# Performance work log

Measured on AMD Instinct MI355X. Metric: run time of the kernel, lower is better.

## Reference

```python
import jax, jax.numpy as jnp
import numpy as np

B, TQ, TK, E, H, DH = 4, 1024, 1024, 1024, 16, 64
EPS = 1e-5

def setup_inputs() -> dict:
    key = jax.random.key(0)
    ks = jax.random.split(key, 16)
    s = 0.02
    return {
        "x": jax.random.normal(ks[0], (B, TQ, E), jnp.float32),
        "encoder_out": jax.random.normal(ks[1], (B, TK, E), jnp.float32),
        "Q1w": jax.random.normal(ks[2], (H, DH, E), jnp.float32) * s,
        "Q1b": jax.random.normal(ks[3], (H, DH), jnp.float32) * s,
        "Q2w": jax.random.normal(ks[4], (H, DH, E), jnp.float32) * s,
        "Q2b": jax.random.normal(ks[5], (H, DH), jnp.float32) * s,
        "K1w": jax.random.normal(ks[6], (H, DH, E), jnp.float32) * s,
        "K1b": jax.random.normal(ks[7], (H, DH), jnp.float32) * s,
        "K2w": jax.random.normal(ks[8], (H, DH, E), jnp.float32) * s,
        "K2b": jax.random.normal(ks[9], (H, DH), jnp.float32) * s,
        "Vw": jax.random.normal(ks[10], (H, DH, E), jnp.float32) * s,
        "Vb": jax.random.normal(ks[11], (H, DH), jnp.float32) * s,
        "lam": jax.random.uniform(ks[12], (H,), jnp.float32, 0.5, 1.0),
        "gn_gamma": jnp.ones((H * DH,), jnp.float32),
        "gn_beta": jnp.zeros((H * DH,), jnp.float32),
        "out_w": jax.random.normal(ks[13], (E, H * DH), jnp.float32) * s,
        "out_b": jax.random.normal(ks[14], (E,), jnp.float32) * s,
    }

def _proj(inp, w, b):
    # inp: [B,T,E], w: [H,DH,E] -> [B,H,T,DH]
    return jnp.einsum('bte,hde->bhtd', inp, w) + b[None, :, None, :]

def reference(x, encoder_out, Q1w, Q1b, Q2w, Q2b, K1w, K1b, K2w, K2b, Vw, Vb,
              lam, gn_gamma, gn_beta, out_w, out_b):
    scale = 1.0 / jnp.sqrt(jnp.float32(DH))
    q1 = _proj(x, Q1w, Q1b)
    q2 = _proj(x, Q2w, Q2b)
    k1 = _proj(encoder_out, K1w, K1b)
    k2 = _proj(encoder_out, K2w, K2b)
    v = _proj(encoder_out, Vw, Vb)
    s1 = jnp.einsum('bhtd,bhsd->bhts', q1, k1) * scale  # [B,H,TQ,TK]
    s2 = jnp.einsum('bhtd,bhsd->bhts', q2, k2) * scale
    w = jax.nn.softmax(s1, axis=-1) - lam[None, :, None, None] * jax.nn.softmax(s2, axis=-1)
    out = jnp.einsum('bhts,bhsd->bhtd', w, v)  # [B,H,TQ,DH]
    # GroupNorm(num_groups=H, channels=H*DH) over [B,C,T]: per (B,H) stats over (T,DH)
    mu = jnp.mean(out, axis=(2, 3), keepdims=True)
    var = jnp.mean(jnp.square(out - mu), axis=(2, 3), keepdims=True)
    normed = (out - mu) * jax.lax.rsqrt(var + EPS)
    g = gn_gamma.reshape(H, DH)[None, :, None, :]
    b_ = gn_beta.reshape(H, DH)[None, :, None, :]
    normed = normed * g + b_
    y = normed.transpose(0, 2, 1, 3).reshape(B, TQ, H * DH)
    return y @ out_w.T + out_b
```

## Files before the change

kernel.cpp:

```cpp
#include <hip/hip_runtime.h>
#include <cmath>

typedef __bf16 bf16_t;
typedef bf16_t bf16x8 __attribute__((ext_vector_type(8)));
typedef bf16_t bf16x4 __attribute__((ext_vector_type(4)));
typedef float  f32x4  __attribute__((ext_vector_type(4)));

#define Bn  4
#define TQn 1024
#define TKn 1024
#define En  1024
#define Hn  16
#define DHn 64

static constexpr float EPSv = 1e-5f;
static constexpr float C_SCALE = 0.18033688011112042f;

#define GLDS16(g, l)                                                         \
    __builtin_amdgcn_global_load_lds(                                        \
        (const __attribute__((address_space(1))) void*)(g),                  \
        (__attribute__((address_space(3))) void*)(l), 16, 0, 0)

__global__ __launch_bounds__(256)
void cvt_all(const float* __restrict__ x, const float* __restrict__ enc,
             const float* __restrict__ q1w, const float* __restrict__ q2w,
             const float* __restrict__ k1w, const float* __restrict__ k2w,
             const float* __restrict__ vw,  const float* __restrict__ outw,
             bf16_t* __restrict__ xb, bf16_t* __restrict__ encb,
             bf16_t* __restrict__ wq, bf16_t* __restrict__ wkv,
             bf16_t* __restrict__ wob)
{
    int idx = blockIdx.x * 256 + threadIdx.x;
    const float* src; bf16_t* dst;
    if      (idx < 1048576) { src = x    + (size_t)idx * 4;              dst = xb   + (size_t)idx * 4; }
    else if (idx < 2097152) { src = enc  + (size_t)(idx - 1048576) * 4;  dst = encb + (size_t)(idx - 1048576) * 4; }
    else if (idx < 2359296) { src = q1w  + (size_t)(idx - 2097152) * 4;  dst = wq   + (size_t)(idx - 2097152) * 4; }
    else if (idx < 2621440) { src = q2w  + (size_t)(idx - 2359296) * 4;  dst = wq   + 1048576 + (size_t)(idx - 2359296) * 4; }
    else if (idx < 2883584) { src = k1w  + (size_t)(idx - 2621440) * 4;  dst = wkv  + (size_t)(idx - 2621440) * 4; }
    else if (idx < 3145728) { src = k2w  + (size_t)(idx - 2883584) * 4;  dst = wkv  + 1048576 + (size_t)(idx - 2883584) * 4; }
    else if (idx < 3407872) { src = vw   + (size_t)(idx - 3145728) * 4;  dst = wkv  + 2097152 + (size_t)(idx - 3145728) * 4; }
    else                    { src = outw + (size_t)(idx - 3407872) * 4;  dst = wob  + (size_t)(idx - 3407872) * 4; }
    float4 v = *(const float4*)src;
    bf16x4 o;
    o[0] = (bf16_t)v.x; o[1] = (bf16_t)v.y; o[2] = (bf16_t)v.z; o[3] = (bf16_t)v.w;
    *(bf16x4*)dst = o;
}

template<int OUTMODE, int BN>
__device__ __forceinline__
void gemm_core(const bf16_t* __restrict__ A, const bf16_t* __restrict__ W,
               const float* __restrict__ bp, void* __restrict__ Cout,
               int K, int blockM, int blockN,
               bf16_t* __restrict__ sA, bf16_t* __restrict__ sB)
{
    constexpr int NJ = BN / 32;
    constexpr int CB = BN / 32;
    const int tid = threadIdx.x;
    const int w = tid >> 6, lane = tid & 63;
    const int q = lane >> 4, r = lane & 15;
    const int wm = w & 1, wn = w >> 1;

    f32x4 acc[4][NJ];
#pragma unroll
    for (int i = 0; i < 4; ++i)
#pragma unroll
        for (int j = 0; j < NJ; ++j) acc[i][j] = (f32x4){0.f, 0.f, 0.f, 0.f};

    for (int k0 = 0; k0 < K; k0 += 64) {
#pragma unroll
        for (int c = 0; c < 4; ++c) {
            const int s = c * 256 + tid;
            const int row = s >> 3;
            const int cg = (s & 7) ^ (row & 7);
            GLDS16(A + (size_t)(blockM + row) * K + k0 + cg * 8, sA + c * 2048 + w * 512);
            if (c < CB)
                GLDS16(W + (size_t)(blockN + row) * K + k0 + cg * 8, sB + c * 2048 + w * 512);
        }
        __syncthreads();
#pragma unroll
        for (int ks = 0; ks < 2; ++ks) {
            bf16x8 a[4], b[NJ];
#pragma unroll
            for (int i = 0; i < 4; ++i) {
                const int row = wm * 64 + i * 16 + r;
                const int g = (ks * 4 + q) ^ (row & 7);
                a[i] = *(const bf16x8*)&sA[row * 64 + g * 8];
            }
#pragma unroll
            for (int j = 0; j < NJ; ++j) {
                const int row = wn * (BN / 2) + j * 16 + r;
                const int g = (ks * 4 + q) ^ (row & 7);
                b[j] = *(const bf16x8*)&sB[row * 64 + g * 8];
            }
#pragma unroll
            for (int i = 0; i < 4; ++i)
#pragma unroll
                for (int j = 0; j < NJ; ++j)
                    acc[i][j] = __builtin_amdgcn_mfma_f32_16x16x32_bf16(a[i], b[j], acc[i][j], 0, 0, 0);
        }
        __syncthreads();
    }

    const int seg = blockN >> 10;
#pragma unroll
    for (int j = 0; j < NJ; ++j) {
        const int n = blockN + wn * (BN / 2) + j * 16 + r;
        const float bv = bp[n & 1023];
#pragma unroll
        for (int i = 0; i < 4; ++i) {
            f32x4 v = acc[i][j];
#pragma unroll
            for (int e = 0; e < 4; ++e) {
                const int m = blockM + wm * 64 + i * 16 + q * 4 + e;
                const float val = v[e] + bv;
                if (OUTMODE == 0) {
                    const int bb = m >> 10, t = m & 1023;
                    const int h = (n >> 6) & 15, d = n & 63;
                    ((bf16_t*)Cout)[((((size_t)seg * 4 + bb) * 16 + h) * 1024 + t) * 64 + d] = (bf16_t)val;
                } else {
                    ((float*)Cout)[(size_t)m * 1024 + n] = val;
                }
            }
        }
    }
}

__global__ __launch_bounds__(256, 3)
void gemm_proj(const bf16_t* __restrict__ xb, const bf16_t* __restrict__ encb,
               const bf16_t* __restrict__ wq, const bf16_t* __restrict__ wkv,
               const float* __restrict__ q1b, const float* __restrict__ q2b,
               const float* __restrict__ k1b, const float* __restrict__ k2b,
               const float* __restrict__ vb,
               bf16_t* __restrict__ q12, bf16_t* __restrict__ k12v)
{
    __shared__ bf16_t sA[128 * 64];
    __shared__ bf16_t sB[128 * 64];
    int bx = blockIdx.x;
    const bf16_t* A; const bf16_t* W; bf16_t* C; const float* bp; int blockN;
    if (bx < 16) {
        A = xb; W = wq; C = q12; blockN = bx << 7;
        bp = (blockN >> 10) ? q2b : q1b;
    } else {
        bx -= 16;
        A = encb; W = wkv; C = k12v; blockN = bx << 7;
        const int seg = blockN >> 10;
        bp = (seg == 0) ? k1b : ((seg == 1) ? k2b : vb);
    }
    gemm_core<0, 128>(A, W, bp, C, 1024, blockIdx.y << 7, blockN, sA, sB);
}

__global__ __launch_bounds__(256, 3)
void gemm_out(const bf16_t* __restrict__ yb, const bf16_t* __restrict__ wob,
              const float* __restrict__ outb, float* __restrict__ out)
{
    __shared__ bf16_t sA[128 * 64];
    __shared__ bf16_t sB[64 * 64];
    gemm_core<1, 64>(yb, wob, outb, out, 1024, blockIdx.y << 7, blockIdx.x << 6, sA, sB);
}

__device__ __forceinline__ void compute_S(const bf16_t* __restrict__ sK,
                                          const bf16x8 (&fQ)[2][2],
                                          f32x4 (&S)[4][2], int q, int r)
{
#pragma unroll
    for (int i = 0; i < 4; ++i)
#pragma unroll
        for (int j = 0; j < 2; ++j) S[i][j] = (f32x4){0.f, 0.f, 0.f, 0.f};
#pragma unroll
    for (int ks = 0; ks < 2; ++ks) {
        bf16x8 fK[4];
#pragma unroll
        for (int i = 0; i < 4; ++i) {
            const int row = i * 16 + r;
            const int g = (ks * 4 + q) ^ (row & 7);
            fK[i] = *(const bf16x8*)&sK[row * 64 + g * 8];
        }
        __builtin_amdgcn_s_setprio(1);
#pragma unroll
        for (int i = 0; i < 4; ++i)
#pragma unroll
            for (int j = 0; j < 2; ++j)
                S[i][j] = __builtin_amdgcn_mfma_f32_16x16x32_bf16(fK[i], fQ[j][ks], S[i][j], 0, 0, 0);
        __builtin_amdgcn_s_setprio(0);
    }
}

__device__ __forceinline__ void softmax_pw(f32x4 (&S)[4][2], bf16_t* __restrict__ sPt,
                                           float (&l)[2], int w, int q, int r)
{
#pragma unroll
    for (int j = 0; j < 2; ++j) {
        const int t = w * 32 + j * 16 + r;
        float part = 0.f;
#pragma unroll
        for (int i = 0; i < 4; ++i) {
            bf16x4 pk;
#pragma unroll
            for (int e = 0; e < 4; ++e) {
                const float p = __builtin_amdgcn_exp2f(S[i][j][e] * C_SCALE);
                part += p;
                pk[e] = (bf16_t)p;
            }
            const int sb = i * 16 + q * 4;
            const int g = (sb >> 3) ^ (t & 7);
            *(bf16x4*)&sPt[t * 64 + g * 8 + (sb & 7)] = pk;
        }
        l[j] += part;
    }
}

__device__ __forceinline__ void pv(const bf16_t* __restrict__ sPt,
                                   const bf16x8 (&fV)[4][2],
                                   f32x4 (&O)[2][4], int w, int q, int r)
{
#pragma unroll
    for (int ks = 0; ks < 2; ++ks) {
        bf16x8 fP[2];
#pragma unroll
        for (int i2 = 0; i2 < 2; ++i2) {
            const int m = w * 32 + i2 * 16 + r;
            const int g = (ks * 4 + q) ^ (m & 7);
            fP[i2] = *(const bf16x8*)&sPt[m * 64 + g * 8];
        }
        __builtin_amdgcn_s_setprio(1);
#pragma unroll
        for (int i2 = 0; i2 < 2; ++i2)
#pragma unroll
            for (int j = 0; j < 4; ++j)
                O[i2][j] = __builtin_amdgcn_mfma_f32_16x16x32_bf16(fP[i2], fV[j][ks], O[i2][j], 0, 0, 0);
        __builtin_amdgcn_s_setprio(0);
    }
}

__global__ __launch_bounds__(256, 2)
void diff_attn_mfma(const bf16_t* __restrict__ q12, const bf16_t* __restrict__ k12v,
                    const float* __restrict__ lam, bf16_t* __restrict__ out,
                    float* __restrict__ stats)
{
    __shared__ bf16_t sK1[2][64 * 64];
    __shared__ bf16_t sK2[2][64 * 64];
    __shared__ bf16_t sVt[64 * 64];
    __shared__ bf16_t sPt1[128 * 64];
    __shared__ bf16_t sPt2[128 * 64];
    __shared__ float  sl1[128], sl2[128];
    __shared__ float  sred[16];

    const int tid = threadIdx.x;
    const int w = tid >> 6, lane = tid & 63;
    const int q = lane >> 4, r = lane & 15;
    const int bh = blockIdx.x, qt = blockIdx.y;
    const float lamv = lam[bh & (Hn - 1)];

    const size_t HT = (size_t)TKn * DHn;
    const bf16_t* q1g = q12 + (size_t)bh * HT + (size_t)qt * 128 * DHn;
    const bf16_t* q2g = q1g + 64 * HT;
    const bf16_t* k1g = k12v + (size_t)bh * HT;
    const bf16_t* k2g = k1g + 64 * HT;
    const bf16_t* vg  = k1g + 128 * HT;

    bf16x8 fQ1[2][2], fQ2[2][2];
#pragma unroll
    for (int j = 0; j < 2; ++j) {
        const int t = w * 32 + j * 16 + r;
#pragma unroll
        for (int ks = 0; ks < 2; ++ks) {
            fQ1[j][ks] = *(const bf16x8*)(q1g + (size_t)t * 64 + ks * 32 + q * 8);
            fQ2[j][ks] = *(const bf16x8*)(q2g + (size_t)t * 64 + ks * 32 + q * 8);
        }
    }

    f32x4 O1[2][4], O2[2][4];
    float l1[2] = {0.f, 0.f}, l2[2] = {0.f, 0.f};
#pragma unroll
    for (int i = 0; i < 2; ++i)
#pragma unroll
        for (int j = 0; j < 4; ++j) { O1[i][j] = (f32x4){0.f,0.f,0.f,0.f}; O2[i][j] = (f32x4){0.f,0.f,0.f,0.f}; }

    {
#pragma unroll
        for (int c = 0; c < 2; ++c) {
            const int s = c * 256 + tid;
            const int row = s >> 3;
            const int cg = (s & 7) ^ (row & 7);
            GLDS16(k1g + row * 64 + cg * 8, &sK1[0][c * 2048 + w * 512]);
            GLDS16(k2g + row * 64 + cg * 8, &sK2[0][c * 2048 + w * 512]);
        }
        bf16x8 v0[2];
#pragma unroll
        for (int rep = 0; rep < 2; ++rep)
            v0[rep] = *(const bf16x8*)(vg + (size_t)lane * 64 + (w * 2 + rep) * 8);
        __syncthreads();
#pragma unroll
        for (int rep = 0; rep < 2; ++rep) {
            const int d0 = (w * 2 + rep) * 8;
#pragma unroll
            for (int i = 0; i < 8; ++i) {
                const int d = d0 + i;
                sVt[d * 64 + (((lane >> 3) ^ i) << 3) + (lane & 7)] = v0[rep][i];
            }
        }
        __syncthreads();
    }

    bf16x8 vr[2];
    for (int st = 0; st < TKn / 64; ++st) {
        const int cur = st & 1;
        if (st < 15) {
            const bf16_t* k1p = k1g + (size_t)(st + 1) * 4096;
            const bf16_t* k2p = k2g + (size_t)(st + 1) * 4096;
#pragma unroll
            for (int c = 0; c < 2; ++c) {
                const int s = c * 256 + tid;
                const int row = s >> 3;
                const int cg = (s & 7) ^ (row & 7);
                GLDS16(k1p + row * 64 + cg * 8, &sK1[cur ^ 1][c * 2048 + w * 512]);
                GLDS16(k2p + row * 64 + cg * 8, &sK2[cur ^ 1][c * 2048 + w * 512]);
            }
            const bf16_t* vp = vg + (size_t)(st + 1) * 4096;
#pragma unroll
            for (int rep = 0; rep < 2; ++rep)
                vr[rep] = *(const bf16x8*)(vp + (size_t)lane * 64 + (w * 2 + rep) * 8);
        }

        {
            f32x4 S[4][2];
            compute_S(sK1[cur], fQ1, S, q, r);
            softmax_pw(S, sPt1, l1, w, q, r);
        }
        {
            f32x4 S[4][2];
            compute_S(sK2[cur], fQ2, S, q, r);
            softmax_pw(S, sPt2, l2, w, q, r);
        }
        bf16x8 fV[4][2];
#pragma unroll
        for (int j = 0; j < 4; ++j)
#pragma unroll
            for (int ks = 0; ks < 2; ++ks) {
                const int d = j * 16 + r;
                const int g = (ks * 4 + q) ^ (d & 7);
                fV[j][ks] = *(const bf16x8*)&sVt[d * 64 + g * 8];
            }
        pv(sPt1, fV, O1, w, q, r);
        pv(sPt2, fV, O2, w, q, r);

        __syncthreads();
        if (st < 15) {
#pragma unroll
            for (int rep = 0; rep < 2; ++rep) {
                const int d0 = (w * 2 + rep) * 8;
#pragma unroll
                for (int i = 0; i < 8; ++i) {
                    const int d = d0 + i;
                    sVt[d * 64 + (((lane >> 3) ^ i) << 3) + (lane & 7)] = vr[rep][i];
                }
            }
            __syncthreads();
        }
    }

#pragma unroll
    for (int j = 0; j < 2; ++j) {
        float v1 = l1[j];
        v1 += __shfl_xor(v1, 16); v1 += __shfl_xor(v1, 32);
        float v2 = l2[j];
        v2 += __shfl_xor(v2, 16); v2 += __shfl_xor(v2, 32);
        if (q == 0) { sl1[w * 32 + j * 16 + r] = v1; sl2[w * 32 + j * 16 + r] = v2; }
    }

    bf16_t* op = out + ((size_t)bh * TQn + (size_t)qt * 128) * DHn;
    float ssum = 0.f, ssq = 0.f;
#pragma unroll
    for (int i2 = 0; i2 < 2; ++i2)
#pragma unroll
        for (int e = 0; e < 4; ++e) {
            const int t = w * 32 + i2 * 16 + q * 4 + e;
            const float inv1 = 1.0f / sl1[t];
            const float inv2 = lamv / sl2[t];
#pragma unroll
            for (int j = 0; j < 4; ++j) {
                const float o = O1[i2][j][e] * inv1 - O2[i2][j][e] * inv2;
                op[(size_t)t * 64 + j * 16 + r] = (bf16_t)o;
                ssum += o;
                ssq += o * o;
            }
        }
#pragma unroll
    for (int d = 1; d < 64; d <<= 1) {
        ssum += __shfl_xor(ssum, d);
        ssq  += __shfl_xor(ssq, d);
    }
    if (lane == 0) { sred[w] = ssum; sred[8 + w] = ssq; }
    __syncthreads();
    if (tid == 0) {
        stats[(bh << 3) + qt]       = sred[0] + sred[1] + sred[2] + sred[3];
        stats[512 + (bh << 3) + qt] = sred[8] + sred[9] + sred[10] + sred[11];
    }
}

__global__ __launch_bounds__(256)
void gn_apply(const bf16_t* __restrict__ attn, const float* __restrict__ stats,
              const float* __restrict__ gamma, const float* __restrict__ beta,
              bf16_t* __restrict__ y)
{
    const int f = blockIdx.x * 256 + threadIdx.x;
    const int d8 = (f & 7) << 3;
    const int t  = (f >> 3) & 1023;
    const int bh = f >> 13;
    const int h  = bh & 15;
    const int b  = bh >> 4;
    const float* p1 = stats + (bh << 3);
    const float* p2 = stats + 512 + (bh << 3);
    float s1 = 0.f, s2 = 0.f;
#pragma unroll
    for (int k = 0; k < 8; ++k) { s1 += p1[k]; s2 += p2[k]; }
    const float mu = s1 * (1.f / 65536.f);
    const float var = s2 * (1.f / 65536.f) - mu * mu;
    const float rstd = rsqrtf(var + EPSv);
    bf16x8 v = *(const bf16x8*)&attn[((size_t)bh << 16) + t * 64 + d8];
    const int c = h * 64 + d8;
    const float* gp = gamma + c;
    const float* bp = beta + c;
    bf16x8 o;
#pragma unroll
    for (int i = 0; i < 8; ++i)
        o[i] = (bf16_t)(((float)v[i] - mu) * rstd * gp[i] + bp[i]);
    *(bf16x8*)&y[((size_t)(b * 1024 + t)) * 1024 + c] = o;
}

extern "C" void kernel_launch(void* const* d_in, const int* in_sizes, int n_in,
                              void* d_out, int out_size, void* d_ws, size_t ws_size,
                              hipStream_t stream)
{
    const float* x    = (const float*)d_in[0];
    const float* enc  = (const float*)d_in[1];
    const float* Q1w  = (const float*)d_in[2];
    const float* Q1b  = (const float*)d_in[3];
    const float* Q2w  = (const float*)d_in[4];
    const float* Q2b  = (const float*)d_in[5];
    const float* K1w  = (const float*)d_in[6];
    const float* K1b  = (const float*)d_in[7];
    const float* K2w  = (const float*)d_in[8];
    const float* K2b  = (const float*)d_in[9];
    const float* Vw   = (const float*)d_in[10];
    const float* Vb   = (const float*)d_in[11];
    const float* lam  = (const float*)d_in[12];
    const float* gng  = (const float*)d_in[13];
    const float* gnb  = (const float*)d_in[14];
    const float* outw = (const float*)d_in[15];
    const float* outb = (const float*)d_in[16];
    float* out = (float*)d_out;

    bf16_t* xb   = (bf16_t*)d_ws;
    bf16_t* encb = xb   + 4194304;
    bf16_t* wq   = encb + 4194304;
    bf16_t* wkv  = wq   + 2097152;
    bf16_t* wob  = wkv  + 3145728;
    bf16_t* q12  = wob  + 1048576;
    bf16_t* k12v = q12  + 8388608;
    bf16_t* attnb= xb;
    bf16_t* yb   = encb;
    float*  stats= (float*)wq;

    cvt_all<<<14336, 256, 0, stream>>>(x, enc, Q1w, Q2w, K1w, K2w, Vw, outw,
                                       xb, encb, wq, wkv, wob);

    gemm_proj<<<dim3(40, 32), 256, 0, stream>>>(xb, encb, wq, wkv,
                                                Q1b, Q2b, K1b, K2b, Vb, q12, k12v);

    diff_attn_mfma<<<dim3(64, 8), 256, 0, stream>>>(q12, k12v, lam, attnb, stats);

    gn_apply<<<2048, 256, 0, stream>>>(attnb, stats, gng, gnb, yb);

    gemm_out<<<dim3(16, 32), 256, 0, stream>>>(yb, wob, outb, out);
}
```

Measured before the change: 252.3 us.

## Use 512-thread attention blocks, shared P buffer, and remapped 64x128 output GEMM

The attention kernel moves to 8 waves per block, each owning 16 query rows, and interleaves S, softmax and PV per branch so a single P buffer in LDS is reused by both branches. The output GEMM switches to 64x128 tiles with a 1-D grid whose block index is remapped so neighbouring blocks on each XCD share A rows, and its occupancy hint rises to 4. The generic gemm_core template is inlined into each kernel. The aim is more waves in flight, less LDS use and better L2 locality. The cost is half the MFMA work per wave in attention and extra synchronisation overhead per block.

```diff
diff --git a/kernel.cpp b/kernel.cpp
--- a/kernel.cpp
+++ b/kernel.cpp
@@ -46,85 +46,6 @@
     *(bf16x4*)dst = o;
 }
 
-template<int OUTMODE, int BN>
-__device__ __forceinline__
-void gemm_core(const bf16_t* __restrict__ A, const bf16_t* __restrict__ W,
-               const float* __restrict__ bp, void* __restrict__ Cout,
-               int K, int blockM, int blockN,
-               bf16_t* __restrict__ sA, bf16_t* __restrict__ sB)
-{
-    constexpr int NJ = BN / 32;
-    constexpr int CB = BN / 32;
-    const int tid = threadIdx.x;
-    const int w = tid >> 6, lane = tid & 63;
-    const int q = lane >> 4, r = lane & 15;
-    const int wm = w & 1, wn = w >> 1;
-
-    f32x4 acc[4][NJ];
-#pragma unroll
-    for (int i = 0; i < 4; ++i)
-#pragma unroll
-        for (int j = 0; j < NJ; ++j) acc[i][j] = (f32x4){0.f, 0.f, 0.f, 0.f};
-
-    for (int k0 = 0; k0 < K; k0 += 64) {
-#pragma unroll
-        for (int c = 0; c < 4; ++c) {
-            const int s = c * 256 + tid;
-            const int row = s >> 3;
-            const int cg = (s & 7) ^ (row & 7);
-            GLDS16(A + (size_t)(blockM + row) * K + k0 + cg * 8, sA + c * 2048 + w * 512);
-            if (c < CB)
-                GLDS16(W + (size_t)(blockN + row) * K + k0 + cg * 8, sB + c * 2048 + w * 512);
-        }
-        __syncthreads();
-#pragma unroll
-        for (int ks = 0; ks < 2; ++ks) {
-            bf16x8 a[4], b[NJ];
-#pragma unroll
-            for (int i = 0; i < 4; ++i) {
-                const int row = wm * 64 + i * 16 + r;
-                const int g = (ks * 4 + q) ^ (row & 7);
-                a[i] = *(const bf16x8*)&sA[row * 64 + g * 8];
-            }
-#pragma unroll
-            for (int j = 0; j < NJ; ++j) {
-                const int row = wn * (BN / 2) + j * 16 + r;
-                const int g = (ks * 4 + q) ^ (row & 7);
-                b[j] = *(const bf16x8*)&sB[row * 64 + g * 8];
-            }
-#pragma unroll
-            for (int i = 0; i < 4; ++i)
-#pragma unroll
-                for (int j = 0; j < NJ; ++j)
-                    acc[i][j] = __builtin_amdgcn_mfma_f32_16x16x32_bf16(a[i], b[j], acc[i][j], 0, 0, 0);
-        }
-        __syncthreads();
-    }
-
-    const int seg = blockN >> 10;
-#pragma unroll
-    for (int j = 0; j < NJ; ++j) {
-        const int n = blockN + wn * (BN / 2) + j * 16 + r;
-        const float bv = bp[n & 1023];
-#pragma unroll
-        for (int i = 0; i < 4; ++i) {
-            f32x4 v = acc[i][j];
-#pragma unroll
-            for (int e = 0; e < 4; ++e) {
-                const int m = blockM + wm * 64 + i * 16 + q * 4 + e;
-                const float val = v[e] + bv;
-                if (OUTMODE == 0) {
-                    const int bb = m >> 10, t = m & 1023;
-                    const int h = (n >> 6) & 15, d = n & 63;
-                    ((bf16_t*)Cout)[((((size_t)seg * 4 + bb) * 16 + h) * 1024 + t) * 64 + d] = (bf16_t)val;
-                } else {
-                    ((float*)Cout)[(size_t)m * 1024 + n] = val;
-                }
-            }
-        }
-    }
-}
-
 __global__ __launch_bounds__(256, 3)
 void gemm_proj(const bf16_t* __restrict__ xb, const bf16_t* __restrict__ encb,
                const bf16_t* __restrict__ wq, const bf16_t* __restrict__ wkv,
@@ -146,26 +67,156 @@
         const int seg = blockN >> 10;
         bp = (seg == 0) ? k1b : ((seg == 1) ? k2b : vb);
     }
-    gemm_core<0, 128>(A, W, bp, C, 1024, blockIdx.y << 7, blockN, sA, sB);
-}
-
-__global__ __launch_bounds__(256, 3)
+    const int blockM = blockIdx.y << 7;
+
+    const int tid = threadIdx.x;
+    const int w = tid >> 6, lane = tid & 63;
+    const int q = lane >> 4, r = lane & 15;
+    const int wm = w & 1, wn = w >> 1;
+
+    f32x4 acc[4][4];
+#pragma unroll
+    for (int i = 0; i < 4; ++i)
+#pragma unroll
+        for (int j = 0; j < 4; ++j) acc[i][j] = (f32x4){0.f, 0.f, 0.f, 0.f};
+
+    for (int k0 = 0; k0 < 1024; k0 += 64) {
+#pragma unroll
+        for (int c = 0; c < 4; ++c) {
+            const int s = c * 256 + tid;
+            const int row = s >> 3;
+            const int cg = (s & 7) ^ (row & 7);
+            GLDS16(A + (size_t)(blockM + row) * 1024 + k0 + cg * 8, sA + c * 2048 + w * 512);
+            GLDS16(W + (size_t)(blockN + row) * 1024 + k0 + cg * 8, sB + c * 2048 + w * 512);
+        }
+        __syncthreads();
+#pragma unroll
+        for (int ks = 0; ks < 2; ++ks) {
+            bf16x8 a[4], b[4];
+#pragma unroll
+            for (int i = 0; i < 4; ++i) {
+                const int row = wm * 64 + i * 16 + r;
+                const int g = (ks * 4 + q) ^ (row & 7);
+                a[i] = *(const bf16x8*)&sA[row * 64 + g * 8];
+            }
+#pragma unroll
+            for (int j = 0; j < 4; ++j) {
+                const int row = wn * 64 + j * 16 + r;
+                const int g = (ks * 4 + q) ^ (row & 7);
+                b[j] = *(const bf16x8*)&sB[row * 64 + g * 8];
+            }
+#pragma unroll
+            for (int i = 0; i < 4; ++i)
+#pragma unroll
+                for (int j = 0; j < 4; ++j)
+                    acc[i][j] = __builtin_amdgcn_mfma_f32_16x16x32_bf16(a[i], b[j], acc[i][j], 0, 0, 0);
+        }
+        __syncthreads();
+    }
+
+    const int seg = blockN >> 10;
+#pragma unroll
+    for (int j = 0; j < 4; ++j) {
+        const int n = blockN + wn * 64 + j * 16 + r;
+        const float bv = bp[n & 1023];
+#pragma unroll
+        for (int i = 0; i < 4; ++i) {
+            f32x4 v = acc[i][j];
+#pragma unroll
+            for (int e = 0; e < 4; ++e) {
+                const int m = blockM + wm * 64 + i * 16 + q * 4 + e;
+                const float val = v[e] + bv;
+                const int bb = m >> 10, t = m & 1023;
+                const int h = (n >> 6) & 15, d = n & 63;
+                ((bf16_t*)C)[((((size_t)seg * 4 + bb) * 16 + h) * 1024 + t) * 64 + d] = (bf16_t)val;
+            }
+        }
+    }
+}
+
+__global__ __launch_bounds__(256, 4)
 void gemm_out(const bf16_t* __restrict__ yb, const bf16_t* __restrict__ wob,
               const float* __restrict__ outb, float* __restrict__ out)
 {
-    __shared__ bf16_t sA[128 * 64];
-    __shared__ bf16_t sB[64 * 64];
-    gemm_core<1, 64>(yb, wob, outb, out, 1024, blockIdx.y << 7, blockIdx.x << 6, sA, sB);
+    __shared__ bf16_t sA[64 * 64];
+    __shared__ bf16_t sB[128 * 64];
+    const int L = blockIdx.x;
+    const int xcd = L & 7, kk = L >> 3;
+    const int blockM = (xcd * 8 + (kk >> 3)) * 64;
+    const int blockN = (kk & 7) * 128;
+
+    const int tid = threadIdx.x;
+    const int w = tid >> 6, lane = tid & 63;
+    const int q = lane >> 4, r = lane & 15;
+
+    f32x4 acc[4][2];
+#pragma unroll
+    for (int i = 0; i < 4; ++i)
+#pragma unroll
+        for (int j = 0; j < 2; ++j) acc[i][j] = (f32x4){0.f, 0.f, 0.f, 0.f};
+
+    for (int k0 = 0; k0 < 1024; k0 += 64) {
+#pragma unroll
+        for (int c = 0; c < 2; ++c) {
+            const int s = c * 256 + tid;
+            const int row = s >> 3;
+            const int cg = (s & 7) ^ (row & 7);
+            GLDS16(yb + (size_t)(blockM + row) * 1024 + k0 + cg * 8, sA + c * 2048 + w * 512);
+        }
+#pragma unroll
+        for (int c = 0; c < 4; ++c) {
+            const int s = c * 256 + tid;
+            const int row = s >> 3;
+            const int cg = (s & 7) ^ (row & 7);
+            GLDS16(wob + (size_t)(blockN + row) * 1024 + k0 + cg * 8, sB + c * 2048 + w * 512);
+        }
+        __syncthreads();
+#pragma unroll
+        for (int ks = 0; ks < 2; ++ks) {
+            bf16x8 a[4], b[2];
+#pragma unroll
+            for (int i = 0; i < 4; ++i) {
+                const int row = i * 16 + r;
+                const int g = (ks * 4 + q) ^ (row & 7);
+                a[i] = *(const bf16x8*)&sA[row * 64 + g * 8];
+            }
+#pragma unroll
+            for (int j = 0; j < 2; ++j) {
+                const int row = w * 32 + j * 16 + r;
+                const int g = (ks * 4 + q) ^ (row & 7);
+                b[j] = *(const bf16x8*)&sB[row * 64 + g * 8];
+            }
+#pragma unroll
+            for (int i = 0; i < 4; ++i)
+#pragma unroll
+                for (int j = 0; j < 2; ++j)
+                    acc[i][j] = __builtin_amdgcn_mfma_f32_16x16x32_bf16(a[i], b[j], acc[i][j], 0, 0, 0);
+        }
+        __syncthreads();
+    }
+
+#pragma unroll
+    for (int j = 0; j < 2; ++j) {
+        const int n = blockN + w * 32 + j * 16 + r;
+        const float bv = outb[n];
+#pragma unroll
+        for (int i = 0; i < 4; ++i) {
+            f32x4 v = acc[i][j];
+#pragma unroll
+            for (int e = 0; e < 4; ++e) {
+                const int m = blockM + i * 16 + q * 4 + e;
+                out[(size_t)m * 1024 + n] = v[e] + bv;
+            }
+        }
+    }
 }
 
 __device__ __forceinline__ void compute_S(const bf16_t* __restrict__ sK,
-                                          const bf16x8 (&fQ)[2][2],
-                                          f32x4 (&S)[4][2], int q, int r)
-{
-#pragma unroll
-    for (int i = 0; i < 4; ++i)
-#pragma unroll
-        for (int j = 0; j < 2; ++j) S[i][j] = (f32x4){0.f, 0.f, 0.f, 0.f};
+                                          const bf16x8 (&fQ)[2],
+                                          f32x4 (&S)[4], int q, int r)
+{
+#pragma unroll
+    for (int i = 0; i < 4; ++i) S[i] = (f32x4){0.f, 0.f, 0.f, 0.f};
 #pragma unroll
     for (int ks = 0; ks < 2; ++ks) {
         bf16x8 fK[4];
@@ -178,61 +229,50 @@
         __builtin_amdgcn_s_setprio(1);
 #pragma unroll
         for (int i = 0; i < 4; ++i)
-#pragma unroll
-            for (int j = 0; j < 2; ++j)
-                S[i][j] = __builtin_amdgcn_mfma_f32_16x16x32_bf16(fK[i], fQ[j][ks], S[i][j], 0, 0, 0);
+            S[i] = __builtin_amdgcn_mfma_f32_16x16x32_bf16(fK[i], fQ[ks], S[i], 0, 0, 0);
         __builtin_amdgcn_s_setprio(0);
     }
 }
 
-__device__ __forceinline__ void softmax_pw(f32x4 (&S)[4][2], bf16_t* __restrict__ sPt,
-                                           float (&l)[2], int w, int q, int r)
-{
-#pragma unroll
-    for (int j = 0; j < 2; ++j) {
-        const int t = w * 32 + j * 16 + r;
-        float part = 0.f;
-#pragma unroll
-        for (int i = 0; i < 4; ++i) {
-            bf16x4 pk;
-#pragma unroll
-            for (int e = 0; e < 4; ++e) {
-                const float p = __builtin_amdgcn_exp2f(S[i][j][e] * C_SCALE);
-                part += p;
-                pk[e] = (bf16_t)p;
-            }
-            const int sb = i * 16 + q * 4;
-            const int g = (sb >> 3) ^ (t & 7);
-            *(bf16x4*)&sPt[t * 64 + g * 8 + (sb & 7)] = pk;
-        }
-        l[j] += part;
-    }
+__device__ __forceinline__ void softmax_pw(f32x4 (&S)[4], bf16_t* __restrict__ sPt,
+                                           float& l, int w, int q, int r)
+{
+    const int t = w * 16 + r;
+    float part = 0.f;
+#pragma unroll
+    for (int i = 0; i < 4; ++i) {
+        bf16x4 pk;
+#pragma unroll
+        for (int e = 0; e < 4; ++e) {
+            const float p = __builtin_amdgcn_exp2f(S[i][e] * C_SCALE);
+            part += p;
+            pk[e] = (bf16_t)p;
+        }
+        const int sb = i * 16 + q * 4;
+        const int g = (sb >> 3) ^ (t & 7);
+        *(bf16x4*)&sPt[t * 64 + g * 8 + (sb & 7)] = pk;
+    }
+    l += part;
 }
 
 __device__ __forceinline__ void pv(const bf16_t* __restrict__ sPt,
                                    const bf16x8 (&fV)[4][2],
-                                   f32x4 (&O)[2][4], int w, int q, int r)
+                                   f32x4 (&O)[4], int w, int q, int r)
 {
 #pragma unroll
     for (int ks = 0; ks < 2; ++ks) {
-        bf16x8 fP[2];
-#pragma unroll
-        for (int i2 = 0; i2 < 2; ++i2) {
-            const int m = w * 32 + i2 * 16 + r;
-            const int g = (ks * 4 + q) ^ (m & 7);
-            fP[i2] = *(const bf16x8*)&sPt[m * 64 + g * 8];
-        }
+        const int m = w * 16 + r;
+        const int g = (ks * 4 + q) ^ (m & 7);
+        bf16x8 fP = *(const bf16x8*)&sPt[m * 64 + g * 8];
         __builtin_amdgcn_s_setprio(1);
 #pragma unroll
-        for (int i2 = 0; i2 < 2; ++i2)
-#pragma unroll
-            for (int j = 0; j < 4; ++j)
-                O[i2][j] = __builtin_amdgcn_mfma_f32_16x16x32_bf16(fP[i2], fV[j][ks], O[i2][j], 0, 0, 0);
+        for (int j = 0; j < 4; ++j)
+            O[j] = __builtin_amdgcn_mfma_f32_16x16x32_bf16(fP, fV[j][ks], O[j], 0, 0, 0);
         __builtin_amdgcn_s_setprio(0);
     }
 }
 
-__global__ __launch_bounds__(256, 2)
+__global__ __launch_bounds__(512, 2)
 void diff_attn_mfma(const bf16_t* __restrict__ q12, const bf16_t* __restrict__ k12v,
                     const float* __restrict__ lam, bf16_t* __restrict__ out,
                     float* __restrict__ stats)
@@ -240,8 +280,7 @@
     __shared__ bf16_t sK1[2][64 * 64];
     __shared__ bf16_t sK2[2][64 * 64];
     __shared__ bf16_t sVt[64 * 64];
-    __shared__ bf16_t sPt1[128 * 64];
-    __shared__ bf16_t sPt2[128 * 64];
+    __shared__ bf16_t sPt[128 * 64];
     __shared__ float  sl1[128], sl2[128];
     __shared__ float  sred[16];
 
@@ -258,80 +297,47 @@
     const bf16_t* k2g = k1g + 64 * HT;
     const bf16_t* vg  = k1g + 128 * HT;
 
-    bf16x8 fQ1[2][2], fQ2[2][2];
-#pragma unroll
-    for (int j = 0; j < 2; ++j) {
-        const int t = w * 32 + j * 16 + r;
+    bf16x8 fQ1[2], fQ2[2];
+    {
+        const int t = w * 16 + r;
 #pragma unroll
         for (int ks = 0; ks < 2; ++ks) {
-            fQ1[j][ks] = *(const bf16x8*)(q1g + (size_t)t * 64 + ks * 32 + q * 8);
-            fQ2[j][ks] = *(const bf16x8*)(q2g + (size_t)t * 64 + ks * 32 + q * 8);
-        }
-    }
-
-    f32x4 O1[2][4], O2[2][4];
-    float l1[2] = {0.f, 0.f}, l2[2] = {0.f, 0.f};
-#pragma unroll
-    for (int i = 0; i < 2; ++i)
-#pragma unroll
-        for (int j = 0; j < 4; ++j) { O1[i][j] = (f32x4){0.f,0.f,0.f,0.f}; O2[i][j] = (f32x4){0.f,0.f,0.f,0.f}; }
+            fQ1[ks] = *(const bf16x8*)(q1g + (size_t)t * 64 + ks * 32 + q * 8);
+            fQ2[ks] = *(const bf16x8*)(q2g + (size_t)t * 64 + ks * 32 + q * 8);
+        }
+    }
+
+    f32x4 O1[4], O2[4];
+    float l1 = 0.f, l2 = 0.f;
+#pragma unroll
+    for (int j = 0; j < 4; ++j) { O1[j] = (f32x4){0.f,0.f,0.f,0.f}; O2[j] = (f32x4){0.f,0.f,0.f,0.f}; }
 
     {
-#pragma unroll
-        for (int c = 0; c < 2; ++c) {
-            const int s = c * 256 + tid;
-            const int row = s >> 3;
-            const int cg = (s & 7) ^ (row & 7);
-            GLDS16(k1g + row * 64 + cg * 8, &sK1[0][c * 2048 + w * 512]);
-            GLDS16(k2g + row * 64 + cg * 8, &sK2[0][c * 2048 + w * 512]);
-        }
-        bf16x8 v0[2];
-#pragma unroll
-        for (int rep = 0; rep < 2; ++rep)
-            v0[rep] = *(const bf16x8*)(vg + (size_t)lane * 64 + (w * 2 + rep) * 8);
-        __syncthreads();
-#pragma unroll
-        for (int rep = 0; rep < 2; ++rep) {
-            const int d0 = (w * 2 + rep) * 8;
-#pragma unroll
-            for (int i = 0; i < 8; ++i) {
-                const int d = d0 + i;
-                sVt[d * 64 + (((lane >> 3) ^ i) << 3) + (lane & 7)] = v0[rep][i];
-            }
-        }
-        __syncthreads();
-    }
-
-    bf16x8 vr[2];
+        const int row = tid >> 3;
+        const int cg = (tid & 7) ^ (row & 7);
+        GLDS16(k1g + row * 64 + cg * 8, &sK1[0][tid * 8]);
+        GLDS16(k2g + row * 64 + cg * 8, &sK2[0][tid * 8]);
+        const int s = tid & 63;
+        bf16x8 v0 = *(const bf16x8*)(vg + (size_t)s * 64 + w * 8);
+#pragma unroll
+        for (int i = 0; i < 8; ++i) {
+            const int d = w * 8 + i;
+            sVt[d * 64 + (((s >> 3) ^ i) << 3) + (s & 7)] = v0[i];
+        }
+        __syncthreads();
+    }
+
+    bf16x8 vr;
     for (int st = 0; st < TKn / 64; ++st) {
         const int cur = st & 1;
         if (st < 15) {
-            const bf16_t* k1p = k1g + (size_t)(st + 1) * 4096;
-            const bf16_t* k2p = k2g + (size_t)(st + 1) * 4096;
-#pragma unroll
-            for (int c = 0; c < 2; ++c) {
-                const int s = c * 256 + tid;
-                const int row = s >> 3;
-                const int cg = (s & 7) ^ (row & 7);
-                GLDS16(k1p + row * 64 + cg * 8, &sK1[cur ^ 1][c * 2048 + w * 512]);
-                GLDS16(k2p + row * 64 + cg * 8, &sK2[cur ^ 1][c * 2048 + w * 512]);
-            }
-            const bf16_t* vp = vg + (size_t)(st + 1) * 4096;
-#pragma unroll
-            for (int rep = 0; rep < 2; ++rep)
-                vr[rep] = *(const bf16x8*)(vp + (size_t)lane * 64 + (w * 2 + rep) * 8);
-        }
-
-        {
-            f32x4 S[4][2];
-            compute_S(sK1[cur], fQ1, S, q, r);
-            softmax_pw(S, sPt1, l1, w, q, r);
-        }
-        {
-            f32x4 S[4][2];
-            compute_S(sK2[cur], fQ2, S, q, r);
-            softmax_pw(S, sPt2, l2, w, q, r);
-        }
+            const int row = tid >> 3;
+            const int cg = (tid & 7) ^ (row & 7);
+            GLDS16(k1g + (size_t)(st + 1) * 4096 + row * 64 + cg * 8, &sK1[cur ^ 1][tid * 8]);
+            GLDS16(k2g + (size_t)(st + 1) * 4096 + row * 64 + cg * 8, &sK2[cur ^ 1][tid * 8]);
+            vr = *(const bf16x8*)(vg + (size_t)(st + 1) * 4096 + (size_t)(tid & 63) * 64 + w * 8);
+        }
+
         bf16x8 fV[4][2];
 #pragma unroll
         for (int j = 0; j < 4; ++j)
@@ -341,50 +347,54 @@
                 const int g = (ks * 4 + q) ^ (d & 7);
                 fV[j][ks] = *(const bf16x8*)&sVt[d * 64 + g * 8];
             }
-        pv(sPt1, fV, O1, w, q, r);
-        pv(sPt2, fV, O2, w, q, r);
+        {
+            f32x4 S[4];
+            compute_S(sK1[cur], fQ1, S, q, r);
+            softmax_pw(S, sPt, l1, w, q, r);
+            pv(sPt, fV, O1, w, q, r);
+        }
+        {
+            f32x4 S[4];
+            compute_S(sK2[cur], fQ2, S, q, r);
+            softmax_pw(S, sPt, l2, w, q, r);
+            pv(sPt, fV, O2, w, q, r);
+        }
 
         __syncthreads();
         if (st < 15) {
-#pragma unroll
-            for (int rep = 0; rep < 2; ++rep) {
-                const int d0 = (w * 2 + rep) * 8;
-#pragma unroll
-                for (int i = 0; i < 8; ++i) {
-                    const int d = d0 + i;
-                    sVt[d * 64 + (((lane >> 3) ^ i) << 3) + (lane & 7)] = vr[rep][i];
-                }
+            const int s = tid & 63;
+#pragma unroll
+            for (int i = 0; i < 8; ++i) {
+                const int d = w * 8 + i;
+                sVt[d * 64 + (((s >> 3) ^ i) << 3) + (s & 7)] = vr[i];
             }
             __syncthreads();
         }
     }
 
-#pragma unroll
-    for (int j = 0; j < 2; ++j) {
-        float v1 = l1[j];
+    {
+        float v1 = l1;
         v1 += __shfl_xor(v1, 16); v1 += __shfl_xor(v1, 32);
-        float v2 = l2[j];
+        float v2 = l2;
         v2 += __shfl_xor(v2, 16); v2 += __shfl_xor(v2, 32);
-        if (q == 0) { sl1[w * 32 + j * 16 + r] = v1; sl2[w * 32 + j * 16 + r] = v2; }
+        if (q == 0) { sl1[w * 16 + r] = v1; sl2[w * 16 + r] = v2; }
     }
 
     bf16_t* op = out + ((size_t)bh * TQn + (size_t)qt * 128) * DHn;
     float ssum = 0.f, ssq = 0.f;
 #pragma unroll
-    for (int i2 = 0; i2 < 2; ++i2)
-#pragma unroll
-        for (int e = 0; e < 4; ++e) {
-            const int t = w * 32 + i2 * 16 + q * 4 + e;
-            const float inv1 = 1.0f / sl1[t];
-            const float inv2 = lamv / sl2[t];
-#pragma unroll
-            for (int j = 0; j < 4; ++j) {
-                const float o = O1[i2][j][e] * inv1 - O2[i2][j][e] * inv2;
-                op[(size_t)t * 64 + j * 16 + r] = (bf16_t)o;
-                ssum += o;
-                ssq += o * o;
-            }
-        }
+    for (int e = 0; e < 4; ++e) {
+        const int t = w * 16 + q * 4 + e;
+        const float inv1 = 1.0f / sl1[t];
+        const float inv2 = lamv / sl2[t];
+#pragma unroll
+        for (int j = 0; j < 4; ++j) {
+            const float o = O1[j][e] * inv1 - O2[j][e] * inv2;
+            op[(size_t)t * 64 + j * 16 + r] = (bf16_t)o;
+            ssum += o;
+            ssq += o * o;
+        }
+    }
 #pragma unroll
     for (int d = 1; d < 64; d <<= 1) {
         ssum += __shfl_xor(ssum, d);
@@ -393,8 +403,11 @@
     if (lane == 0) { sred[w] = ssum; sred[8 + w] = ssq; }
     __syncthreads();
     if (tid == 0) {
-        stats[(bh << 3) + qt]       = sred[0] + sred[1] + sred[2] + sred[3];
-        stats[512 + (bh << 3) + qt] = sred[8] + sred[9] + sred[10] + sred[11];
+        float a = 0.f, b = 0.f;
+#pragma unroll
+        for (int k = 0; k < 8; ++k) { a += sred[k]; b += sred[8 + k]; }
+        stats[(bh << 3) + qt]       = a;
+        stats[512 + (bh << 3) + qt] = b;
     }
 }
 
@@ -468,9 +481,9 @@
     gemm_proj<<<dim3(40, 32), 256, 0, stream>>>(xb, encb, wq, wkv,
                                                 Q1b, Q2b, K1b, K2b, Vb, q12, k12v);
 
-    diff_attn_mfma<<<dim3(64, 8), 256, 0, stream>>>(q12, k12v, lam, attnb, stats);
+    diff_attn_mfma<<<dim3(64, 8), 512, 0, stream>>>(q12, k12v, lam, attnb, stats);
 
     gn_apply<<<2048, 256, 0, stream>>>(attnb, stats, gng, gnb, yb);
 
-    gemm_out<<<dim3(16, 32), 256, 0, stream>>>(yb, wob, outb, out);
-}
+    gemm_out<<<512, 256, 0, stream>>>(yb, wob, outb, out);
+}
```

Result: no change. 251.2 us (-0.4%).
